# Kernel tuning notes

Hardware: AMD Instinct MI355X
Metric: run time of the kernel (lower is better)

Reference implementation:

```python
import jax, jax.numpy as jnp
import numpy as np

T, S, N, E, H, FF = 1024, 2048, 4, 1024, 16, 4096
HD = E // H
EPS = 1e-5


def layer_norm(x, g, b):
    mu = jnp.mean(x, axis=-1, keepdims=True)
    var = jnp.mean(jnp.square(x - mu), axis=-1, keepdims=True)
    return (x - mu) / jnp.sqrt(var + EPS) * g + b


def mha(q_in, k_in, v_in, w_in, b_in, w_out, b_out):
    # q_in: (T,N,E), k_in/v_in: (S,N,E); matches torch F.linear with (3E,E) weight
    t, n, e = q_in.shape
    s = k_in.shape[0]
    wq, wk, wv = jnp.split(w_in, 3, axis=0)
    bq, bk, bv = jnp.split(b_in, 3)
    q = (q_in @ wq.T + bq) * (HD ** -0.5)
    k = k_in @ wk.T + bk
    v = v_in @ wv.T + bv
    # (L,N,E) -> (N*H, L, HD)
    q = q.reshape(t, n * H, HD).transpose(1, 0, 2)
    k = k.reshape(s, n * H, HD).transpose(1, 0, 2)
    v = v.reshape(s, n * H, HD).transpose(1, 0, 2)
    attn = jax.nn.softmax(jnp.einsum('bth,bsh->bts', q, k), axis=-1)
    out = jnp.einsum('bts,bsh->bth', attn, v)  # (N*H, T, HD)
    out = out.transpose(1, 0, 2).reshape(t, n, e)
    return out @ w_out.T + b_out


def setup_inputs() -> dict:
    key = jax.random.key(0)
    ks = jax.random.split(key, 16)
    p = lambda k, shape: jax.random.normal(k, shape, dtype=jnp.float32) * 0.02
    return {
        'tgt': jax.random.normal(ks[0], (T, N, E), dtype=jnp.float32),
        'memory': jax.random.normal(ks[1], (S, N, E), dtype=jnp.float32),
        'sa_w_in': p(ks[2], (3 * E, E)), 'sa_b_in': jnp.zeros((3 * E,), jnp.float32),
        'sa_w_out': p(ks[3], (E, E)), 'sa_b_out': jnp.zeros((E,), jnp.float32),
        'ca_w_in': p(ks[4], (3 * E, E)), 'ca_b_in': jnp.zeros((3 * E,), jnp.float32),
        'ca_w_out': p(ks[5], (E, E)), 'ca_b_out': jnp.zeros((E,), jnp.float32),
        'w1': p(ks[6], (FF, E)), 'b1': jnp.zeros((FF,), jnp.float32),
        'w2': p(ks[7], (E, FF)), 'b2': jnp.zeros((E,), jnp.float32),
        'ln1_g': jnp.ones((E,), jnp.float32), 'ln1_b': jnp.zeros((E,), jnp.float32),
        'ln2_g': jnp.ones((E,), jnp.float32), 'ln2_b': jnp.zeros((E,), jnp.float32),
        'ln3_g': jnp.ones((E,), jnp.float32), 'ln3_b': jnp.zeros((E,), jnp.float32),
    }


def reference(tgt, memory, sa_w_in, sa_b_in, sa_w_out, sa_b_out,
              ca_w_in, ca_b_in, ca_w_out, ca_b_out,
              w1, b1, w2, b2, ln1_g, ln1_b, ln2_g, ln2_b, ln3_g, ln3_b):
    # self-attention block (post-LN residual); dropout = identity (eval mode)
    tgt2 = mha(tgt, tgt, tgt, sa_w_in, sa_b_in, sa_w_out, sa_b_out)
    x = layer_norm(tgt + tgt2, ln1_g, ln1_b)
    # cross-attention block
    tgt2 = mha(x, memory, memory, ca_w_in, ca_b_in, ca_w_out, ca_b_out)
    x = layer_norm(x + tgt2, ln2_g, ln2_b)
    # FFN with relu
    tgt2 = jax.nn.relu(x @ w1.T + b1) @ w2.T + b2
    return layer_norm(x + tgt2, ln3_g, ln3_b)
```

## Files before the change

kernel.cpp:

```cpp
#include <hip/hip_runtime.h>


typedef __bf16 bf16x8 __attribute__((ext_vector_type(8)));
typedef float  f32x4  __attribute__((ext_vector_type(4)));
typedef float  f32x16 __attribute__((ext_vector_type(16)));

#define T_  1024
#define S_  2048
#define NB_ 4
#define E_  1024
#define H_  16
#define HD_ 64
#define FF_ 4096
#define M1_ (T_*NB_)
#define M2_ (S_*NB_)
#define LOG2E 1.44269504088896f

__device__ __forceinline__ unsigned short f2bf(float f){
  unsigned int u = __builtin_bit_cast(unsigned int, f);
  u += 0x7fffu + ((u>>16)&1u);
  return (unsigned short)(u>>16);
}
__device__ __forceinline__ float bf2f(unsigned short h){
  unsigned int u = ((unsigned int)h)<<16;
  return __builtin_bit_cast(float, u);
}

__device__ __forceinline__ void gload16(unsigned short* l, const unsigned short* g){
  __builtin_amdgcn_global_load_lds(
      (const __attribute__((address_space(1))) unsigned int*)g,
      (__attribute__((address_space(3))) unsigned int*)l, 16, 0, 0);
}

struct CvtSeg { const float* s; unsigned short* d; int n4; };
struct CvtArgs { CvtSeg seg[8]; int blk_end[8]; };
__global__ __launch_bounds__(256) void f2b_multi_k(CvtArgs a){
  const int b = blockIdx.x;
  int si = 0;
  #pragma unroll
  for (int i=0;i<8;i++) if (b >= a.blk_end[i]) si = i+1;
  const int base = si ? a.blk_end[si-1] : 0;
  const int i4 = (b - base)*256 + threadIdx.x;
  if (i4 >= a.seg[si].n4) return;
  float4 f = ((const float4*)a.seg[si].s)[i4];
  union { unsigned short u[4]; uint2 v; } t;
  t.u[0]=f2bf(f.x); t.u[1]=f2bf(f.y); t.u[2]=f2bf(f.z); t.u[3]=f2bf(f.w);
  ((uint2*)a.seg[si].d)[i4] = t.v;
}

template<int FLAGS, int BN>
__global__ __launch_bounds__(256) void gemm_k(
    const unsigned short* __restrict__ A, int lda,
    const unsigned short* __restrict__ B, int ldb,
    const float* __restrict__ bias,
    const float* __restrict__ res,
    unsigned short* __restrict__ Cb, float* __restrict__ Cf,
    int M, int N, int K)
{
  constexpr int NW = BN/32;
  __shared__ unsigned short a_sh[128*64];
  __shared__ unsigned short b_sh[BN*64];
  const int tid  = threadIdx.x;
  const int wave = tid>>6;
  const int lane = tid&63;
  const int l15 = lane&15, l4 = lane>>4;
  const int row0 = blockIdx.x*128, col0 = blockIdx.y*BN;
  const int wm = (wave>>1)*64, wn = (wave&1)*(BN/2);

  const int lrow = tid>>3;
  const int scol = ((tid&7) ^ (lrow&7)) << 3;
  const int dst8 = (tid&7) << 3;

  f32x4 acc[4][NW] = {};

  for (int k0=0; k0<K; k0+=64){
    const unsigned short* ga = A + (size_t)(row0+lrow)*lda + k0 + scol;
    const unsigned short* gb = B + (size_t)(col0+lrow)*ldb + k0 + scol;
    #pragma unroll
    for (int i=0;i<4;i++)
      gload16(&a_sh[(lrow + i*32)*64 + dst8], ga + (size_t)(i*32)*lda);
    #pragma unroll
    for (int i=0;i<BN/32;i++)
      gload16(&b_sh[(lrow + i*32)*64 + dst8], gb + (size_t)(i*32)*ldb);
    __syncthreads();
    #pragma unroll
    for (int kk=0;kk<2;kk++){
      const int sw = (((kk<<2)|l4) ^ (l15&7)) << 3;
      bf16x8 af[4], bfr[NW];
      #pragma unroll
      for (int m=0;m<4;m++)  af[m]  = *(const bf16x8*)&a_sh[(wm + m*16 + l15)*64 + sw];
      #pragma unroll
      for (int n=0;n<NW;n++) bfr[n] = *(const bf16x8*)&b_sh[(wn + n*16 + l15)*64 + sw];
      #pragma unroll
      for (int m=0;m<4;m++)
        #pragma unroll
        for (int n=0;n<NW;n++)
          acc[m][n] = __builtin_amdgcn_mfma_f32_16x16x32_bf16(af[m], bfr[n], acc[m][n], 0,0,0);
    }
    __syncthreads();
  }

  #pragma unroll
  for (int m=0;m<4;m++){
    #pragma unroll
    for (int r=0;r<4;r++){
      const int rr = row0 + wm + m*16 + l4*4 + r;
      #pragma unroll
      for (int n=0;n<NW;n++){
        const int cc = col0 + wn + n*16 + l15;
        float v = acc[m][n][r] + bias[cc];
        if (FLAGS & 1) v = fmaxf(v, 0.f);
        if (FLAGS & 2) v += res[(size_t)rr*N + cc];
        if (FLAGS & 4) Cb[(size_t)rr*N + cc] = f2bf(v);
        if (FLAGS & 8) Cf[(size_t)rr*N + cc] = v;
      }
    }
  }
}

template<int BN>
__global__ __launch_bounds__(256) void gemm_splitk_k(
    const unsigned short* __restrict__ A, int lda,
    const unsigned short* __restrict__ B, int ldb,
    const float* __restrict__ bias,
    const float* __restrict__ res,
    float* __restrict__ P0, float* __restrict__ P1,
    int M, int N, int K)
{
  constexpr int NW = BN/32;
  __shared__ unsigned short a_sh[128*64];
  __shared__ unsigned short b_sh[BN*64];
  const int tid  = threadIdx.x;
  const int wave = tid>>6;
  const int lane = tid&63;
  const int l15 = lane&15, l4 = lane>>4;
  const int row0 = blockIdx.x*128, col0 = blockIdx.y*BN;
  const int wm = (wave>>1)*64, wn = (wave&1)*(BN/2);
  const int z = blockIdx.z;
  const int kh = K>>1;
  const int kbeg = z*kh;

  const int lrow = tid>>3;
  const int scol = ((tid&7) ^ (lrow&7)) << 3;
  const int dst8 = (tid&7) << 3;

  f32x4 acc[4][NW] = {};

  for (int k0=kbeg; k0<kbeg+kh; k0+=64){
    const unsigned short* ga = A + (size_t)(row0+lrow)*lda + k0 + scol;
    const unsigned short* gb = B + (size_t)(col0+lrow)*ldb + k0 + scol;
    #pragma unroll
    for (int i=0;i<4;i++)
      gload16(&a_sh[(lrow + i*32)*64 + dst8], ga + (size_t)(i*32)*lda);
    #pragma unroll
    for (int i=0;i<BN/32;i++)
      gload16(&b_sh[(lrow + i*32)*64 + dst8], gb + (size_t)(i*32)*ldb);
    __syncthreads();
    #pragma unroll
    for (int kk=0;kk<2;kk++){
      const int sw = (((kk<<2)|l4) ^ (l15&7)) << 3;
      bf16x8 af[4], bfr[NW];
      #pragma unroll
      for (int m=0;m<4;m++)  af[m]  = *(const bf16x8*)&a_sh[(wm + m*16 + l15)*64 + sw];
      #pragma unroll
      for (int n=0;n<NW;n++) bfr[n] = *(const bf16x8*)&b_sh[(wn + n*16 + l15)*64 + sw];
      #pragma unroll
      for (int m=0;m<4;m++)
        #pragma unroll
        for (int n=0;n<NW;n++)
          acc[m][n] = __builtin_amdgcn_mfma_f32_16x16x32_bf16(af[m], bfr[n], acc[m][n], 0,0,0);
    }
    __syncthreads();
  }

  float* out = z ? P1 : P0;
  #pragma unroll
  for (int m=0;m<4;m++){
    #pragma unroll
    for (int r=0;r<4;r++){
      const int rr = row0 + wm + m*16 + l4*4 + r;
      #pragma unroll
      for (int n=0;n<NW;n++){
        const int cc = col0 + wn + n*16 + l15;
        float v = acc[m][n][r];
        if (!z) v += bias[cc] + res[(size_t)rr*N + cc];
        out[(size_t)rr*N + cc] = v;
      }
    }
  }
}

template<int BN>
__global__ __launch_bounds__(256) void gemm_scat_k(
    const unsigned short* __restrict__ A, int lda,
    const unsigned short* __restrict__ B, int ldb,
    const float* __restrict__ bias,
    unsigned short* __restrict__ qb, unsigned short* __restrict__ kb,
    unsigned short* __restrict__ vtb,
    int M, int N, int K, int nq, int nk, int Lq, int Lkv, float qscale)
{
  constexpr int NW = BN/32;
  constexpr int SMEM_ELEMS = (BN==128) ? (128*132) : (128*64 + BN*64);
  __shared__ unsigned short smem[SMEM_ELEMS];
  unsigned short* a_sh = smem;
  unsigned short* b_sh = smem + 128*64;
  const int tid  = threadIdx.x;
  const int wave = tid>>6, lane = tid&63;
  const int l15 = lane&15, l4 = lane>>4;
  const int row0 = blockIdx.x*128, col0 = blockIdx.y*BN;
  const int wm = (wave>>1)*64, wn = (wave&1)*(BN/2);

  const int lrow = tid>>3;
  const int scol = ((tid&7) ^ (lrow&7)) << 3;
  const int dst8 = (tid&7) << 3;

  f32x4 acc[4][NW] = {};

  for (int k0=0; k0<K; k0+=64){
    const unsigned short* ga = A + (size_t)(row0+lrow)*lda + k0 + scol;
    const unsigned short* gb = B + (size_t)(col0+lrow)*ldb + k0 + scol;
    #pragma unroll
    for (int i=0;i<4;i++)
      gload16(&a_sh[(lrow + i*32)*64 + dst8], ga + (size_t)(i*32)*lda);
    #pragma unroll
    for (int i=0;i<BN/32;i++)
      gload16(&b_sh[(lrow + i*32)*64 + dst8], gb + (size_t)(i*32)*ldb);
    __syncthreads();
    #pragma unroll
    for (int kk=0;kk<2;kk++){
      const int sw = (((kk<<2)|l4) ^ (l15&7)) << 3;
      bf16x8 af[4], bfr[NW];
      #pragma unroll
      for (int m=0;m<4;m++)  af[m]  = *(const bf16x8*)&a_sh[(wm + m*16 + l15)*64 + sw];
      #pragma unroll
      for (int n=0;n<NW;n++) bfr[n] = *(const bf16x8*)&b_sh[(wn + n*16 + l15)*64 + sw];
      #pragma unroll
      for (int m=0;m<4;m++)
        #pragma unroll
        for (int n=0;n<NW;n++)
          acc[m][n] = __builtin_amdgcn_mfma_f32_16x16x32_bf16(af[m], bfr[n], acc[m][n], 0,0,0);
    }
    __syncthreads();
  }

  if (col0 < nq + nk){
    const bool isq = (col0 < nq);
    unsigned short* dst = isq ? qb : kb;
    const int  base  = isq ? 0 : nq;
    const int  L     = isq ? Lq : Lkv;
    const float scale = isq ? qscale : 1.0f;
    #pragma unroll
    for (int m=0;m<4;m++){
      #pragma unroll
      for (int r=0;r<4;r++){
        const int rr = row0 + wm + m*16 + l4*4 + r;
        const int t = rr>>2, nn = rr&3;
        #pragma unroll
        for (int n=0;n<NW;n++){
          const int cc = col0 + wn + n*16 + l15;
          const int e = cc - base, h = e>>6, d = e&63;
          const float v = (acc[m][n][r] + bias[cc]) * scale;
          dst[((size_t)(nn*H_ + h)*L + t)*HD_ + d] = f2bf(v);
        }
      }
    }
  } else if constexpr (BN == 128){
    unsigned short* cT = smem;
    #pragma unroll
    for (int m=0;m<4;m++){
      const int tl = ((wm + m*16)>>2) + l4;
      #pragma unroll
      for (int n=0;n<4;n++){
        const int ccl = wn + n*16 + l15;
        const float bi = bias[col0 + ccl];
        #pragma unroll
        for (int r=0;r<4;r++)
          cT[ccl*132 + r*32 + tl] = f2bf(acc[m][n][r] + bi);
      }
    }
    __syncthreads();
    const int t0 = row0>>2;
    const int tl4 = tid&7, c5 = tid>>3;
    const int voff = nq + nk;
    #pragma unroll
    for (int i=0;i<16;i++){
      const int combo = i*32 + c5;
      const int nn = combo&3, ccl = combo>>2;
      const int e = col0 + ccl - voff, h = e>>6, d = e&63;
      const uint2 val = *(const uint2*)&cT[ccl*132 + nn*32 + tl4*4];
      *(uint2*)(vtb + (size_t)((nn*H_ + h)*HD_ + d)*Lkv + t0 + tl4*4) = val;
    }
  }
}

template<bool PARTIAL>
__global__ __launch_bounds__(256) void attn_k(
    const unsigned short* __restrict__ qb, const unsigned short* __restrict__ kb,
    const unsigned short* __restrict__ vtb,
    unsigned short* __restrict__ o_out, float* __restrict__ l_out,
    int T, int S, int s_count)
{
  __shared__ unsigned short k_sh[64*64];
  __shared__ unsigned short v_sh[64*64];
  __shared__ float bc_sh[4][32];
  const int tid  = threadIdx.x;
  const int wave = tid>>6, lane = tid&63;
  const int l31  = lane&31;
  const int hv   = lane>>5;
  const int bh   = blockIdx.x;
  const int z    = blockIdx.z;
  const int s_begin = z * s_count;
  const int q0   = blockIdx.y*128 + wave*32;
  const size_t qbase = (size_t)bh*T*HD_;
  const size_t kbase = (size_t)bh*S*HD_;
  const size_t vbase = (size_t)bh*HD_*S;

  const int strow = tid>>3;
  const int stch  = tid&7;

  bf16x8 qf[4];
  #pragma unroll
  for (int p=0;p<4;p++)
    qf[p] = *(const bf16x8*)(qb + qbase + (size_t)(q0 + l31)*HD_ + p*16 + hv*8);

  f32x16 o0 = {}, o1 = {};
  float l_run = 0.f;

  for (int s0=s_begin; s0<s_begin+s_count; s0+=64){
    #pragma unroll
    for (int i=0;i<2;i++){
      const int row = strow + 32*i;
      const int sc  = ((stch ^ (row&7)) << 3);
      gload16(&k_sh[row*64 + (stch<<3)], kb  + kbase + (size_t)(s0+row)*HD_ + sc);
      gload16(&v_sh[row*64 + (stch<<3)], vtb + vbase + (size_t)row*S + s0 + sc);
    }
    __syncthreads();

    f32x16 sc0 = {}, sc1 = {};
    #pragma unroll
    for (int p=0;p<4;p++){
      const int slot = 2*p + hv;
      bf16x8 kf0 = *(const bf16x8*)&k_sh[(l31     )*64 + ((slot ^ (l31&7))<<3)];
      bf16x8 kf1 = *(const bf16x8*)&k_sh[(l31 + 32)*64 + ((slot ^ (l31&7))<<3)];
      sc0 = __builtin_amdgcn_mfma_f32_32x32x16_bf16(kf0, qf[p], sc0, 0,0,0);
      sc1 = __builtin_amdgcn_mfma_f32_32x32x16_bf16(kf1, qf[p], sc1, 0,0,0);
    }

    float rs = 0.f;
    #pragma unroll
    for (int r=0;r<16;r++){
      sc0[r] = __builtin_amdgcn_exp2f(sc0[r]);
      sc1[r] = __builtin_amdgcn_exp2f(sc1[r]);
      rs += sc0[r] + sc1[r];
    }
    rs += __shfl_xor(rs, 32);
    l_run += rs;

    bf16x8 pa[4];
    #pragma unroll
    for (int ks=0;ks<4;ks++){
      const int base = 8*(ks&1);
      unsigned pkA0, pkA1, pkB0, pkB1;
      if (ks < 2){
        asm("v_cvt_pk_bf16_f32 %0, %1, %2" : "=v"(pkA0) : "v"(sc0[base+0]), "v"(sc0[base+1]));
        asm("v_cvt_pk_bf16_f32 %0, %1, %2" : "=v"(pkA1) : "v"(sc0[base+2]), "v"(sc0[base+3]));
        asm("v_cvt_pk_bf16_f32 %0, %1, %2" : "=v"(pkB0) : "v"(sc0[base+4]), "v"(sc0[base+5]));
        asm("v_cvt_pk_bf16_f32 %0, %1, %2" : "=v"(pkB1) : "v"(sc0[base+6]), "v"(sc0[base+7]));
      } else {
        asm("v_cvt_pk_bf16_f32 %0, %1, %2" : "=v"(pkA0) : "v"(sc1[base+0]), "v"(sc1[base+1]));
        asm("v_cvt_pk_bf16_f32 %0, %1, %2" : "=v"(pkA1) : "v"(sc1[base+2]), "v"(sc1[base+3]));
        asm("v_cvt_pk_bf16_f32 %0, %1, %2" : "=v"(pkB0) : "v"(sc1[base+4]), "v"(sc1[base+5]));
        asm("v_cvt_pk_bf16_f32 %0, %1, %2" : "=v"(pkB1) : "v"(sc1[base+6]), "v"(sc1[base+7]));
      }
      const unsigned send0 = hv ? pkA0 : pkB0;
      const unsigned send1 = hv ? pkA1 : pkB1;
      const unsigned recv0 = __shfl_xor(send0, 32);
      const unsigned recv1 = __shfl_xor(send1, 32);
      union { unsigned w[4]; bf16x8 v; } u;
      u.w[0] = hv ? recv0 : pkA0;
      u.w[1] = hv ? recv1 : pkA1;
      u.w[2] = hv ? pkB0  : recv0;
      u.w[3] = hv ? pkB1  : recv1;
      pa[ks] = u.v;
    }

    #pragma unroll
    for (int ks=0;ks<4;ks++){
      const int slot = 2*ks + hv;
      bf16x8 vf0 = *(const bf16x8*)&v_sh[(l31     )*64 + ((slot ^ (l31&7))<<3)];
      bf16x8 vf1 = *(const bf16x8*)&v_sh[(l31 + 32)*64 + ((slot ^ ((l31+32)&7))<<3)];
      o0 = __builtin_amdgcn_mfma_f32_32x32x16_bf16(pa[ks], vf0, o0, 0,0,0);
      o1 = __builtin_amdgcn_mfma_f32_32x32x16_bf16(pa[ks], vf1, o1, 0,0,0);
    }
    __syncthreads();
  }

  if constexpr (PARTIAL){
    const size_t obase = (size_t)(z*64 + bh)*T;
    #pragma unroll
    for (int r=0;r<16;r++){
      const int qr = (r&3) + 8*(r>>2) + 4*hv;
      unsigned short* op = o_out + (obase + q0 + qr)*HD_;
      op[l31]      = f2bf(o0[r]);
      op[l31 + 32] = f2bf(o1[r]);
    }
    if (hv == 0) l_out[obase + q0 + l31] = l_run;
  } else {
    bc_sh[wave][l31] = 1.f / l_run;
    const int nb = bh>>4, hh = bh&15;
    #pragma unroll
    for (int r=0;r<16;r++){
      const int qr  = (r&3) + 8*(r>>2) + 4*hv;
      const float inv = bc_sh[wave][qr];
      const int t = q0 + qr;
      unsigned short* op = o_out + ((size_t)t*NB_ + nb)*E_ + hh*HD_;
      op[l31]      = f2bf(o0[r]*inv);
      op[l31 + 32] = f2bf(o1[r]*inv);
    }
  }
}

__global__ __launch_bounds__(256) void comb_k(
    const unsigned short* __restrict__ opart, const float* __restrict__ lpart,
    unsigned short* __restrict__ outb, int T)
{
  const int bh = blockIdx.y;
  const int t  = blockIdx.x*4 + (threadIdx.x>>6);
  const int d  = threadIdx.x&63;
  const size_t half = (size_t)64*T;
  const size_t row  = (size_t)bh*T + t;
  const float o = bf2f(opart[row*HD_ + d]) + bf2f(opart[(half + row)*HD_ + d]);
  const float l = lpart[row] + lpart[half + row];
  const int nb = bh>>4, hh = bh&15;
  outb[((size_t)t*NB_ + nb)*E_ + hh*HD_ + d] = f2bf(o / l);
}

__global__ __launch_bounds__(256) void ln_k(
    const float* __restrict__ p0, const float* __restrict__ p1,
    const float* __restrict__ g, const float* __restrict__ bb,
    float* __restrict__ of, unsigned short* __restrict__ ob)
{
  const int row = blockIdx.x, tid = threadIdx.x;
  const size_t base = (size_t)row*E_;
  float v[4];
  #pragma unroll
  for (int i=0;i<4;i++){
    const int col = tid + 256*i;
    v[i] = p0[base + col] + p1[base + col];
  }
  float s  = v[0]+v[1]+v[2]+v[3];
  float s2 = v[0]*v[0]+v[1]*v[1]+v[2]*v[2]+v[3]*v[3];
  #pragma unroll
  for (int off=32; off>0; off>>=1){
    s  += __shfl_down(s, off);
    s2 += __shfl_down(s2, off);
  }
  __shared__ float red[8];
  if ((tid&63)==0){ red[tid>>6] = s; red[4+(tid>>6)] = s2; }
  __syncthreads();
  s  = red[0]+red[1]+red[2]+red[3];
  s2 = red[4]+red[5]+red[6]+red[7];
  const float mu   = s * (1.f/E_);
  const float var  = s2 * (1.f/E_) - mu*mu;
  const float rstd = rsqrtf(var + 1e-5f);
  #pragma unroll
  for (int i=0;i<4;i++){
    const int col = tid + 256*i;
    const float y = (v[i]-mu)*rstd*g[col] + bb[col];
    if (of) of[base + col] = y;
    if (ob) ob[base + col] = f2bf(y);
  }
}

extern "C" void kernel_launch(void* const* d_in, const int* in_sizes, int n_in,
                              void* d_out, int out_size, void* d_ws, size_t ws_size,
                              hipStream_t stream)
{
  const float* tgt      = (const float*)d_in[0];
  const float* mem      = (const float*)d_in[1];
  const float* sa_w_in  = (const float*)d_in[2];
  const float* sa_b_in  = (const float*)d_in[3];
  const float* sa_w_out = (const float*)d_in[4];
  const float* sa_b_out = (const float*)d_in[5];
  const float* ca_w_in  = (const float*)d_in[6];
  const float* ca_b_in  = (const float*)d_in[7];
  const float* ca_w_out = (const float*)d_in[8];
  const float* ca_b_out = (const float*)d_in[9];
  const float* w1 = (const float*)d_in[10];
  const float* b1 = (const float*)d_in[11];
  const float* w2 = (const float*)d_in[12];
  const float* b2 = (const float*)d_in[13];
  const float* ln1_g=(const float*)d_in[14]; const float* ln1_b=(const float*)d_in[15];
  const float* ln2_g=(const float*)d_in[16]; const float* ln2_b=(const float*)d_in[17];
  const float* ln3_g=(const float*)d_in[18]; const float* ln3_b=(const float*)d_in[19];

  char* ws = (char*)d_ws;
  size_t off = 0;
  auto alloc = [&](size_t bytes)->char* {
    char* p = ws + off; off += (bytes + 255) & ~(size_t)255; return p;
  };
  unsigned short* w_sa_in_b  = (unsigned short*)alloc((size_t)3*E_*E_*2);
  unsigned short* w_sa_out_b = (unsigned short*)alloc((size_t)E_*E_*2);
  unsigned short* w_ca_in_b  = (unsigned short*)alloc((size_t)3*E_*E_*2);
  unsigned short* w_ca_out_b = (unsigned short*)alloc((size_t)E_*E_*2);
  unsigned short* w1_b  = (unsigned short*)alloc((size_t)FF_*E_*2);
  unsigned short* w2_b  = (unsigned short*)alloc((size_t)E_*FF_*2);
  unsigned short* tgt_b = (unsigned short*)alloc((size_t)M1_*E_*2);
  unsigned short* mem_b = (unsigned short*)alloc((size_t)M2_*E_*2);
  unsigned short* qbuf  = (unsigned short*)alloc((size_t)64*T_*HD_*2);
  unsigned short* kbuf  = (unsigned short*)alloc((size_t)64*S_*HD_*2);
  unsigned short* vtbuf = (unsigned short*)alloc((size_t)64*S_*HD_*2);
  unsigned short* cbuf  = (unsigned short*)alloc((size_t)M1_*FF_*2);
  unsigned short* atto  = (unsigned short*)alloc((size_t)M1_*E_*2);
  unsigned short* opart = (unsigned short*)alloc((size_t)2*64*T_*HD_*2);
  float*          lpart = (float*)alloc((size_t)2*64*T_*4);
  float* resf = (float*)alloc((size_t)M1_*E_*4);
  float* xf   = (float*)alloc((size_t)M1_*E_*4);
  unsigned short* xb = (unsigned short*)alloc((size_t)M1_*E_*2);
  (void)ws_size; (void)in_sizes; (void)n_in; (void)out_size;

  float* P1 = (float*)opart;

  const float QSCALE = 0.125f * LOG2E;

  {
    CvtArgs a;
    const float* srcs[8] = {tgt, mem, sa_w_in, sa_w_out, ca_w_in, ca_w_out, w1, w2};
    unsigned short* dsts[8] = {tgt_b, mem_b, w_sa_in_b, w_sa_out_b, w_ca_in_b, w_ca_out_b, w1_b, w2_b};
    size_t ns[8] = {(size_t)M1_*E_, (size_t)M2_*E_, (size_t)3*E_*E_, (size_t)E_*E_,
                    (size_t)3*E_*E_, (size_t)E_*E_, (size_t)FF_*E_, (size_t)E_*FF_};
    int blk = 0;
    for (int i=0;i<8;i++){
      a.seg[i].s = srcs[i]; a.seg[i].d = dsts[i]; a.seg[i].n4 = (int)(ns[i]/4);
      blk += (a.seg[i].n4 + 255)/256;
      a.blk_end[i] = blk;
    }
    f2b_multi_k<<<blk, 256, 0, stream>>>(a);
  }

  gemm_scat_k<128><<<dim3(M1_/128, (3*E_)/128), 256, 0, stream>>>(
      tgt_b, E_, w_sa_in_b, E_, sa_b_in, qbuf, kbuf, vtbuf,
      M1_, 3*E_, E_, E_, E_, T_, T_, QSCALE);
  attn_k<false><<<dim3(64, T_/128, 1), 256, 0, stream>>>(
      qbuf, kbuf, vtbuf, atto, nullptr, T_, T_, T_);
  gemm_splitk_k<64><<<dim3(M1_/128, E_/64, 2), 256, 0, stream>>>(
      atto, E_, w_sa_out_b, E_, sa_b_out, tgt, resf, P1, M1_, E_, E_);
  ln_k<<<M1_, 256, 0, stream>>>(resf, P1, ln1_g, ln1_b, xf, xb);

  gemm_scat_k<128><<<dim3(M2_/128, (2*E_)/128), 256, 0, stream>>>(
      mem_b, E_, w_ca_in_b + (size_t)E_*E_, E_, ca_b_in + E_, nullptr, kbuf, vtbuf,
      M2_, 2*E_, E_, 0, E_, T_, S_, QSCALE);
  gemm_scat_k<64><<<dim3(M1_/128, E_/64), 256, 0, stream>>>(
      xb, E_, w_ca_in_b, E_, ca_b_in, qbuf, nullptr, nullptr,
      M1_, E_, E_, E_, 0, T_, S_, QSCALE);
  attn_k<true><<<dim3(64, T_/128, 2), 256, 0, stream>>>(
      qbuf, kbuf, vtbuf, opart, lpart, T_, S_, S_/2);
  comb_k<<<dim3(T_/4, 64), 256, 0, stream>>>(opart, lpart, atto, T_);
  gemm_splitk_k<64><<<dim3(M1_/128, E_/64, 2), 256, 0, stream>>>(
      atto, E_, w_ca_out_b, E_, ca_b_out, xf, resf, P1, M1_, E_, E_);
  ln_k<<<M1_, 256, 0, stream>>>(resf, P1, ln2_g, ln2_b, xf, xb);

  gemm_k<5,128><<<dim3(M1_/128, FF_/128), 256, 0, stream>>>(
      xb, E_, w1_b, E_, b1, nullptr, cbuf, nullptr, M1_, FF_, E_);
  gemm_splitk_k<64><<<dim3(M1_/128, E_/64, 2), 256, 0, stream>>>(
      cbuf, FF_, w2_b, FF_, b2, xf, resf, P1, M1_, E_, FF_);
  ln_k<<<M1_, 256, 0, stream>>>(resf, P1, ln3_g, ln3_b, (float*)d_out, nullptr);
}
```

Measured before the change: 414.9 us.

## Double-buffer K/V tiles in attention and use permlane32 swaps

The attention kernel now keeps two LDS buffers for K and V and prefetches the next 64-key tile while computing on the current one, using explicit vmcnt waits and raw barriers in place of __syncthreads. Cross-half lane exchanges switch from shfl_xor to v_permlane32_swap, and the MFMA sections are wrapped in s_setprio. The aim is to hide global-load latency behind compute and cut shuffle overhead. In exchange LDS use doubles, which may lower occupancy, and the hand-written waitcnt/barrier ordering is fragile.

```diff
diff --git a/kernel.cpp b/kernel.cpp
--- a/kernel.cpp
+++ b/kernel.cpp
@@ -30,6 +30,10 @@
   __builtin_amdgcn_global_load_lds(
       (const __attribute__((address_space(1))) unsigned int*)g,
       (__attribute__((address_space(3))) unsigned int*)l, 16, 0, 0);
+}
+
+__device__ __forceinline__ void perm32swap(unsigned &a, unsigned &b){
+  asm("v_permlane32_swap_b32 %0, %1" : "+v"(a), "+v"(b));
 }
 
 struct CvtSeg { const float* s; unsigned short* d; int n4; };
@@ -300,8 +304,8 @@
     unsigned short* __restrict__ o_out, float* __restrict__ l_out,
     int T, int S, int s_count)
 {
-  __shared__ unsigned short k_sh[64*64];
-  __shared__ unsigned short v_sh[64*64];
+  __shared__ unsigned short k_sh[2][64*64];
+  __shared__ unsigned short v_sh[2][64*64];
   __shared__ float bc_sh[4][32];
   const int tid  = threadIdx.x;
   const int wave = tid>>6, lane = tid&63;
@@ -317,6 +321,19 @@
 
   const int strow = tid>>3;
   const int stch  = tid&7;
+  const int sc_sw = (stch ^ (strow&7)) << 3;
+  const int dst8  = stch<<3;
+
+  {
+    const unsigned short* gk = kb  + kbase + (size_t)s_begin*HD_;
+    const unsigned short* gv = vtb + vbase + s_begin;
+    #pragma unroll
+    for (int i=0;i<2;i++){
+      const int row = strow + 32*i;
+      gload16(&k_sh[0][row*64 + dst8], gk + (size_t)row*HD_ + sc_sw);
+      gload16(&v_sh[0][row*64 + dst8], gv + (size_t)row*S   + sc_sw);
+    }
+  }
 
   bf16x8 qf[4];
   #pragma unroll
@@ -326,25 +343,38 @@
   f32x16 o0 = {}, o1 = {};
   float l_run = 0.f;
 
+  int cur = 0;
   for (int s0=s_begin; s0<s_begin+s_count; s0+=64){
-    #pragma unroll
-    for (int i=0;i<2;i++){
-      const int row = strow + 32*i;
-      const int sc  = ((stch ^ (row&7)) << 3);
-      gload16(&k_sh[row*64 + (stch<<3)], kb  + kbase + (size_t)(s0+row)*HD_ + sc);
-      gload16(&v_sh[row*64 + (stch<<3)], vtb + vbase + (size_t)row*S + s0 + sc);
-    }
-    __syncthreads();
+    if (s0 + 64 < s_begin + s_count){
+      const int nxt = cur^1;
+      const unsigned short* gk = kb  + kbase + (size_t)(s0+64)*HD_;
+      const unsigned short* gv = vtb + vbase + (s0+64);
+      #pragma unroll
+      for (int i=0;i<2;i++){
+        const int row = strow + 32*i;
+        gload16(&k_sh[nxt][row*64 + dst8], gk + (size_t)row*HD_ + sc_sw);
+        gload16(&v_sh[nxt][row*64 + dst8], gv + (size_t)row*S   + sc_sw);
+      }
+      asm volatile("s_waitcnt vmcnt(4)" ::: "memory");
+    } else {
+      asm volatile("s_waitcnt vmcnt(0)" ::: "memory");
+    }
+    __builtin_amdgcn_s_barrier();
+
+    const unsigned short* ksh = k_sh[cur];
+    const unsigned short* vsh = v_sh[cur];
 
     f32x16 sc0 = {}, sc1 = {};
+    __builtin_amdgcn_s_setprio(1);
     #pragma unroll
     for (int p=0;p<4;p++){
       const int slot = 2*p + hv;
-      bf16x8 kf0 = *(const bf16x8*)&k_sh[(l31     )*64 + ((slot ^ (l31&7))<<3)];
-      bf16x8 kf1 = *(const bf16x8*)&k_sh[(l31 + 32)*64 + ((slot ^ (l31&7))<<3)];
+      bf16x8 kf0 = *(const bf16x8*)&ksh[(l31     )*64 + ((slot ^ (l31&7))<<3)];
+      bf16x8 kf1 = *(const bf16x8*)&ksh[(l31 + 32)*64 + ((slot ^ (l31&7))<<3)];
       sc0 = __builtin_amdgcn_mfma_f32_32x32x16_bf16(kf0, qf[p], sc0, 0,0,0);
       sc1 = __builtin_amdgcn_mfma_f32_32x32x16_bf16(kf1, qf[p], sc1, 0,0,0);
     }
+    __builtin_amdgcn_s_setprio(0);
 
     float rs = 0.f;
     #pragma unroll
@@ -353,8 +383,11 @@
       sc1[r] = __builtin_amdgcn_exp2f(sc1[r]);
       rs += sc0[r] + sc1[r];
     }
-    rs += __shfl_xor(rs, 32);
-    l_run += rs;
+    {
+      unsigned ra = __builtin_bit_cast(unsigned, rs), rb = ra;
+      perm32swap(ra, rb);
+      l_run += rs + __builtin_bit_cast(float, hv ? ra : rb);
+    }
 
     bf16x8 pa[4];
     #pragma unroll
@@ -372,27 +405,26 @@
         asm("v_cvt_pk_bf16_f32 %0, %1, %2" : "=v"(pkB0) : "v"(sc1[base+4]), "v"(sc1[base+5]));
         asm("v_cvt_pk_bf16_f32 %0, %1, %2" : "=v"(pkB1) : "v"(sc1[base+6]), "v"(sc1[base+7]));
       }
-      const unsigned send0 = hv ? pkA0 : pkB0;
-      const unsigned send1 = hv ? pkA1 : pkB1;
-      const unsigned recv0 = __shfl_xor(send0, 32);
-      const unsigned recv1 = __shfl_xor(send1, 32);
+      perm32swap(pkA0, pkB0);
+      perm32swap(pkA1, pkB1);
       union { unsigned w[4]; bf16x8 v; } u;
-      u.w[0] = hv ? recv0 : pkA0;
-      u.w[1] = hv ? recv1 : pkA1;
-      u.w[2] = hv ? pkB0  : recv0;
-      u.w[3] = hv ? pkB1  : recv1;
+      u.w[0] = pkA0; u.w[1] = pkA1; u.w[2] = pkB0; u.w[3] = pkB1;
       pa[ks] = u.v;
     }
 
+    __builtin_amdgcn_s_setprio(1);
     #pragma unroll
     for (int ks=0;ks<4;ks++){
       const int slot = 2*ks + hv;
-      bf16x8 vf0 = *(const bf16x8*)&v_sh[(l31     )*64 + ((slot ^ (l31&7))<<3)];
-      bf16x8 vf1 = *(const bf16x8*)&v_sh[(l31 + 32)*64 + ((slot ^ ((l31+32)&7))<<3)];
+      bf16x8 vf0 = *(const bf16x8*)&vsh[(l31     )*64 + ((slot ^ (l31&7))<<3)];
+      bf16x8 vf1 = *(const bf16x8*)&vsh[(l31 + 32)*64 + ((slot ^ (l31&7))<<3)];
       o0 = __builtin_amdgcn_mfma_f32_32x32x16_bf16(pa[ks], vf0, o0, 0,0,0);
       o1 = __builtin_amdgcn_mfma_f32_32x32x16_bf16(pa[ks], vf1, o1, 0,0,0);
     }
-    __syncthreads();
+    __builtin_amdgcn_s_setprio(0);
+
+    __builtin_amdgcn_s_barrier();
+    cur ^= 1;
   }
 
   if constexpr (PARTIAL){
```

Result: faster. 406.0 us (-2.1%).
